# Kernel tuning notes

Measured on AMD Instinct MI355X. Metric: run time of the kernel, lower is better.

Reference implementation:

```python
import jax, jax.numpy as jnp
import numpy as np

B, N, T, D, DG, DS, NC = 16, 64, 256, 64, 64, 9, 2

def _pe(times, d, max_len):
    # PositionalEncodingTF: timescales = max_len ** linspace(0,1,d//2)
    ts = jnp.asarray(max_len ** np.linspace(0.0, 1.0, d // 2), jnp.float32)
    st = times[..., None] / ts
    return jnp.concatenate([jnp.sin(st), jnp.cos(st)], -1)

def _ln(h, g, b):
    m = h.mean(-1, keepdims=True)
    v = ((h - m) ** 2).mean(-1, keepdims=True)
    return (h - m) * jax.lax.rsqrt(v + 1e-5) * g + b

def setup_inputs():
    key = jax.random.key(0)
    ks = jax.random.split(key, 40)
    s = 0.02
    value = jax.random.normal(ks[0], (B, T, N))
    obs = (jax.random.uniform(ks[1], (B, T, N)) < 0.5).astype(jnp.float32)
    times = jnp.sort(jax.random.uniform(ks[2], (B, T)) * T, axis=1)
    F = D + 2 * DG  # per-node GRU input feature size [x_t, h, time_enc]
    return dict(
        x=jnp.concatenate([value, obs, times[..., None]], -1),
        nufft=jax.random.normal(ks[3], (B, 2, T, N)),
        delta_t=jax.random.uniform(ks[4], (B, T)) * 0.1,
        static=jax.random.normal(ks[5], (B, DS)),
        lengths=jax.random.randint(ks[6], (B,), 1, T + 1),
        proj_w=jax.random.normal(ks[7], (2, D)) * s, proj_b=jnp.zeros(D),
        Wqkv=jax.random.normal(ks[8], (D, 3 * D)) * s, bqkv=jnp.zeros(3 * D),
        Wo=jax.random.normal(ks[9], (D, D)) * s, bo=jnp.zeros(D),
        ln1_g=jnp.ones(D), ln1_b=jnp.zeros(D),
        W1=jax.random.normal(ks[10], (D, D)) * s, b1=jnp.zeros(D),
        W2=jax.random.normal(ks[11], (D, D)) * s, b2=jnp.zeros(D),
        ln2_g=jnp.ones(D), ln2_b=jnp.zeros(D),
        WQ_f=jax.random.normal(ks[12], (T, T)) * 0.05,
        WK_f=jax.random.normal(ks[13], (T, T)) * 0.05,
        Wz=jax.random.normal(ks[14], (2 * F, DG)) * s, bz=jnp.zeros(DG),
        Wr=jax.random.normal(ks[15], (2 * F, DG)) * s, br=jnp.zeros(DG),
        Wc=jax.random.normal(ks[16], (2 * F, DG)) * s, bc=jnp.zeros(DG),
        Wfin=jax.random.normal(ks[17], (DG,)) * s, bfin=jnp.zeros(()),
        We=jax.random.normal(ks[18], (DS, N)) * s, be=jnp.zeros(N),
        Wc1=jax.random.normal(ks[19], (2 * N, 200)) * s, bc1=jnp.zeros(200),
        Wc2=jax.random.normal(ks[20], (200, NC)) * s, bc2=jnp.zeros(NC),
    )

def _forward(x, nufft, delta_t, static, lengths, proj_w, proj_b, Wqkv, bqkv, Wo, bo,
             ln1_g, ln1_b, W1, b1, W2, b2, ln2_g, ln2_b, WQ_f, WK_f,
             Wz, bz, Wr, br, Wc, bc, Wfin, bfin, We, be, Wc1, bc1, Wc2, bc2):
    lengths = jnp.maximum(lengths, 1)
    value = x[:, :, :N].transpose(0, 2, 1)          # (B,N,T)
    obs = x[:, :, N:2 * N].transpose(0, 2, 1)       # (B,N,T) observation mask
    times = x[:, :, -1]                              # (B,T)
    # Conv2d(2->D, 1x1) input projection == per-element linear over [value, mask]
    feat = jnp.stack([value, obs], -1) @ proj_w + proj_b   # (B,N,T,D)
    pe1 = _pe(times, D, T)                           # (B,T,D)
    tin = feat + pe1[:, None]                        # (B,N,T,D)
    # single-head transformer encoder layer (post-norm, relu FFN, eval: no dropout)
    qkv = tin @ Wqkv + bqkv
    q, k, v = jnp.split(qkv, 3, -1)
    scores = jnp.einsum('bnqd,bnkd->bnqk', q, k) / jnp.sqrt(jnp.float32(D))
    kpad = jnp.arange(T)[None, :] >= lengths[:, None]      # (B,T) key padding
    scores = jnp.where(kpad[:, None, None, :], -1e9, scores)
    attn = jax.nn.softmax(scores, -1)
    ao = jnp.einsum('bnqk,bnkd->bnqd', attn, v) @ Wo + bo
    h1 = _ln(tin + ao, ln1_g, ln1_b)
    ff = jax.nn.relu(h1 @ W1 + b1) @ W2 + b2
    tout = _ln(h1 + ff, ln2_g, ln2_b)
    m = obs[..., None]
    x_tat = m * tin + (1.0 - m) * tout               # masked blend (B,N,T,D)
    # Variable_Attention_layer on nufft channel 1: relu-score softmax attention
    xf = nufft[:, 1].transpose(0, 2, 1)              # (B,N,T)
    S = jax.nn.relu(jnp.einsum('bnt,bmt->bnm', xf @ WQ_f, xf @ WK_f)) / jnp.sqrt(jnp.float32(T))
    A = jax.nn.softmax(S, -1).mean(0)                # (N,N)
    A = 0.5 * (A + A.T)
    sm = jax.nn.softmax(A, -1)
    A = 0.5 * (sm + sm.T)
    pe2 = _pe(times, DG, T)                          # (B,T,DG)
    # graph-conv GRU over time (CGRNN) with delta_t decay + length masking
    def stepf(h, inputs):
        xt, tet, dtt, t = inputs                     # (B,N,D),(B,DG),(B,),()
        h = h * jnp.exp(-jax.nn.relu(dtt))[:, None, None]
        te = jnp.broadcast_to(tet[:, None, :], (h.shape[0], N, DG))
        inp = jnp.concatenate([xt, h, te], -1)
        gin = jnp.concatenate([inp, jnp.einsum('nm,bmf->bnf', A, inp)], -1)
        z = jax.nn.sigmoid(gin @ Wz + bz)
        r = jax.nn.sigmoid(gin @ Wr + br)
        inc = jnp.concatenate([xt, r * h, te], -1)
        cin = jnp.concatenate([inc, jnp.einsum('nm,bmf->bnf', A, inc)], -1)
        c = jnp.tanh(cin @ Wc + bc)
        hn = z * h + (1.0 - z) * c
        h = jnp.where((t < lengths)[:, None, None], hn, h)
        return h, None
    h0 = jnp.zeros((x.shape[0], N, DG), x.dtype)
    xs = (x_tat.transpose(2, 0, 1, 3), pe2.transpose(1, 0, 2), delta_t.T, jnp.arange(T))
    hT, _ = jax.lax.scan(stepf, h0, xs)
    out = hT @ Wfin + bfin                           # final 1x1 conv -> (B,N)
    emb = static @ We + be                           # (B,N)
    hcl = jax.nn.relu(jnp.concatenate([out, emb], -1) @ Wc1 + bc1)
    return hcl @ Wc2 + bc2                           # (B,NC)

def reference(x, nufft, delta_t, static, lengths, proj_w, proj_b, Wqkv, bqkv, Wo, bo,
              ln1_g, ln1_b, W1, b1, W2, b2, ln2_g, ln2_b, WQ_f, WK_f,
              Wz, bz, Wr, br, Wc, bc, Wfin, bfin, We, be, Wc1, bc1, Wc2, bc2):
    return _forward(x, nufft, delta_t, static, lengths, proj_w, proj_b, Wqkv, bqkv, Wo, bo,
                    ln1_g, ln1_b, W1, b1, W2, b2, ln2_g, ln2_b, WQ_f, WK_f,
                    Wz, bz, Wr, br, Wc, bc, Wfin, bfin, We, be, Wc1, bc1, Wc2, bc2)
```

## Files before the change

### kernel.cpp

```cpp
#include <hip/hip_runtime.h>
#include <hip/hip_bf16.h>
#include <cmath>

#define DEV __device__ __forceinline__

typedef short s16x8 __attribute__((ext_vector_type(8)));
typedef short s16x4 __attribute__((ext_vector_type(4)));
typedef float f32x4 __attribute__((ext_vector_type(4)));

DEV unsigned short f2bu(float x){
  __hip_bfloat16 h = __float2bfloat16(x);
  return *reinterpret_cast<unsigned short*>(&h);
}
DEV float bs2f(unsigned short v){ return __uint_as_float(((unsigned)v)<<16); }
DEV float bs2f(short v){ return bs2f((unsigned short)v); }

DEV int swzo(int row, int col){
  return (row*128 + ((col*2) ^ ((row&7)<<4))) >> 1;
}
DEV s16x8 ldfrag(const short* tile, int t16, int lane, int kk){
  int row = t16 + (lane & 15);
  int c0  = (kk<<5) + ((lane>>4)<<3);
  int off = (row*128 + ((c0<<1) ^ ((row&7)<<4))) >> 1;
  return *(const s16x8*)(tile + off);
}
DEV int swzv(int d, int t){
  return (d*512 + ((t*2) ^ ((d&7)<<4))) >> 1;
}

__global__ void k0_prep(const float* __restrict__ Wqkv, const float* __restrict__ Wo,
                        const float* __restrict__ W1, const float* __restrict__ W2,
                        const float* __restrict__ Wz, const float* __restrict__ Wr,
                        const float* __restrict__ Wc,
                        short* __restrict__ Wqkv_t, short* __restrict__ Wo_t,
                        short* __restrict__ W1_t, short* __restrict__ W2_t,
                        short* __restrict__ Wg_t)
{
  int t = blockIdx.x*256 + threadIdx.x;
  if (t < 12288){ int nn=t>>6, k=t&63; Wqkv_t[t]=(short)f2bu(Wqkv[k*192+nn]); }
  else if (t < 16384){ int e=t-12288; int nn=e>>6,k=e&63; Wo_t[e]=(short)f2bu(Wo[k*64+nn]); }
  else if (t < 20480){ int e=t-16384; int nn=e>>6,k=e&63; W1_t[e]=(short)f2bu(W1[k*64+nn]); }
  else if (t < 24576){ int e=t-20480; int nn=e>>6,k=e&63; W2_t[e]=(short)f2bu(W2[k*64+nn]); }
  else if (t < 49152){
    int e=t-24576;
    int g=e>>13, rem=e&8191, s=rem>>12, rem2=rem&4095, c=rem2>>6, k=rem2&63;
    const float* Wg = (g==0)?Wz:((g==1)?Wr:Wc);
    Wg_t[e] = (short)f2bu(Wg[((s?192:0)+k)*64 + c]);
  }
}

__global__ void k1_pe_u(const float* __restrict__ x, const float* __restrict__ delta_t,
                        const float* __restrict__ Wz, const float* __restrict__ bz,
                        const float* __restrict__ Wr, const float* __restrict__ br,
                        const float* __restrict__ Wc, const float* __restrict__ bc,
                        float* __restrict__ pe, float* __restrict__ U, float* __restrict__ decay)
{
  const int bt = blockIdx.x;
  const int d  = threadIdx.x;
  __shared__ float pes[64];
  float tmv = x[(size_t)bt*129 + 128];
  int j = d & 31;
  float ts = exp2f((float)j * (8.0f/31.0f));
  float st = tmv / ts;
  float v = (d < 32) ? sinf(st) : cosf(st);
  pes[d] = v;
  pe[(size_t)bt*64 + d] = v;
  __syncthreads();
  float a0=bz[d], a1=0.f, a2=br[d], a3=0.f, a4=bc[d], a5=0.f;
  for (int k=0;k<64;k++){
    float p = pes[k];
    a0 = fmaf(p, Wz[(128+k)*64+d], a0);
    a1 = fmaf(p, Wz[(320+k)*64+d], a1);
    a2 = fmaf(p, Wr[(128+k)*64+d], a2);
    a3 = fmaf(p, Wr[(320+k)*64+d], a3);
    a4 = fmaf(p, Wc[(128+k)*64+d], a4);
    a5 = fmaf(p, Wc[(320+k)*64+d], a5);
  }
  float* u = U + (size_t)bt*384;
  u[d]=a0; u[64+d]=a1; u[128+d]=a2; u[192+d]=a3; u[256+d]=a4; u[320+d]=a5;
  if (d==0) decay[bt] = expf(-fmaxf(delta_t[bt], 0.f));
}

__global__ void k2a_qfkf(const float* __restrict__ nufft, const float* __restrict__ WQf,
                         const float* __restrict__ WKf, float* __restrict__ qf, float* __restrict__ kf)
{
  const int bn = blockIdx.x, b = bn>>6, n = bn&63;
  const int u = threadIdx.x;
  __shared__ float xs[256];
  xs[u] = nufft[ ((((size_t)b*2)+1)*256 + u)*64 + n ];
  __syncthreads();
  float aq=0.f, ak=0.f;
  for (int t=0;t<256;t++){
    float xv = xs[t];
    aq = fmaf(xv, WQf[t*256+u], aq);
    ak = fmaf(xv, WKf[t*256+u], ak);
  }
  qf[(size_t)bn*256+u]=aq;
  kf[(size_t)bn*256+u]=ak;
}

__launch_bounds__(256, 1)
__global__ void k2b_soft(const float* __restrict__ qf, const float* __restrict__ kf,
                         float* __restrict__ soft)
{
  const int b = blockIdx.x, tid = threadIdx.x;
  __shared__ float qs[64*257];
  __shared__ float ksh[64*257];
  __shared__ float Ss[64*65];
  const float* qb = qf + ((size_t)b<<14);
  const float* kb = kf + ((size_t)b<<14);
  for (int e=tid; e<16384; e+=256){
    int r=e>>8, c=e&255;
    qs[r*257+c]=qb[e];
    ksh[r*257+c]=kb[e];
  }
  __syncthreads();
  const int n = tid>>2, m0 = (tid&3)<<4;
  float acc[16];
  #pragma unroll
  for (int i=0;i<16;i++) acc[i]=0.f;
  for (int t=0;t<256;t++){
    float qv = qs[n*257+t];
    #pragma unroll
    for (int i=0;i<16;i++) acc[i] = fmaf(qv, ksh[(m0+i)*257+t], acc[i]);
  }
  #pragma unroll
  for (int i=0;i<16;i++) Ss[n*65+m0+i] = fmaxf(acc[i],0.f)*(1.f/16.f);
  __syncthreads();
  if (tid < 64){
    float mx=-1e30f;
    for (int m=0;m<64;m++) mx=fmaxf(mx, Ss[tid*65+m]);
    float s=0.f;
    for (int m=0;m<64;m++) s += expf(Ss[tid*65+m]-mx);
    float inv=1.f/s;
    for (int m=0;m<64;m++) soft[((size_t)b<<12)+(tid<<6)+m] = expf(Ss[tid*65+m]-mx)*inv;
  }
}

__global__ void k2c_A(const float* __restrict__ soft, short* __restrict__ Abf,
                      float* __restrict__ rs_out)
{
  const int tid = threadIdx.x;
  __shared__ float A0[64*65];
  __shared__ float A1[64*65];
  for (int e=tid; e<4096; e+=256){
    int nn=e>>6, mm=e&63;
    float s=0.f;
    #pragma unroll
    for (int b=0;b<16;b++) s += soft[((size_t)b<<12)+e];
    A0[nn*65+mm] = s*(1.f/16.f);
  }
  __syncthreads();
  for (int e=tid; e<4096; e+=256){
    int nn=e>>6, mm=e&63;
    A1[nn*65+mm] = 0.5f*(A0[nn*65+mm]+A0[mm*65+nn]);
  }
  __syncthreads();
  if (tid < 64){
    float mx=-1e30f;
    for (int m=0;m<64;m++) mx=fmaxf(mx, A1[tid*65+m]);
    float s=0.f;
    for (int m=0;m<64;m++) s += expf(A1[tid*65+m]-mx);
    float inv=1.f/s;
    for (int m=0;m<64;m++) A0[tid*65+m] = expf(A1[tid*65+m]-mx)*inv;
  }
  __syncthreads();
  for (int e=tid; e<4096; e+=256){
    int nn=e>>6, mm=e&63;
    float a = 0.5f*(A0[nn*65+mm]+A0[mm*65+nn]);
    A1[nn*65+mm] = a;
    Abf[e] = (short)f2bu(a);
  }
  __syncthreads();
  if (tid < 64){
    float s=0.f;
    for (int m=0;m<64;m++) s += A1[tid*65+m];
    rs_out[tid]=s;
  }
}

__launch_bounds__(512, 1)
__global__ void k3_former(const float* __restrict__ x, const float* __restrict__ pe_g,
    const float* __restrict__ proj_w, const float* __restrict__ proj_b,
    const short* __restrict__ Wqkv_t, const float* __restrict__ bqkv,
    const short* __restrict__ Wo_t, const float* __restrict__ bo,
    const float* __restrict__ ln1g, const float* __restrict__ ln1b,
    const short* __restrict__ W1_t, const float* __restrict__ b1,
    const short* __restrict__ W2_t, const float* __restrict__ b2,
    const float* __restrict__ ln2g, const float* __restrict__ ln2b,
    const int* __restrict__ lengths, unsigned short* __restrict__ xtat)
{
  const int bn = blockIdx.x, b = bn>>6, n = bn&63;
  const int tid = threadIdx.x, w = tid>>6, lane = tid&63;
  const int l15 = lane&15, lhi = lane>>4;
  __shared__ short tp_s[16384];
  __shared__ short q_s[16384];
  __shared__ short k_s[16384];
  __shared__ short v_t[16384];
  __shared__ float valr[256], obsr[256];

// ... 125 lines not shown
      v += __shfl_xor(v,1); v += __shfl_xor(v,2); v += __shfl_xor(v,4); v += __shfl_xor(v,8);
      inv[j][i]=1.f/v;
    }

  #pragma unroll
  for (int j=0;j<2;j++){
    const int rt=w+(j<<3);
    if (rt < LT){
      const int rb=(rt<<4)+(lhi<<2);
      #pragma unroll
      for (int dt=0;dt<4;dt++)
        #pragma unroll
        for (int i=0;i<4;i++)
          q_s[swzo(rb+i,(dt<<4)+l15)] = (short)f2bu(Oac[j][dt][i]*inv[j][i]);
    }
  }
  __syncthreads();

  f32x4 h1[2][4];
  #pragma unroll
  for (int j=0;j<2;j++){
    const int rt=w+(j<<3);
    if (rt < LT){
      s16x8 a0=ldfrag(q_s, rt<<4, lane, 0);
      s16x8 a1=ldfrag(q_s, rt<<4, lane, 1);
      const int rb=(rt<<4)+(lhi<<2);
      #pragma unroll
      for (int dt=0;dt<4;dt++){
        const int col=(dt<<4)+l15;
        const short* wb = Wo_t + (col<<6) + (lhi<<3);
        s16x8 b0=*(const s16x8*)wb, b1v=*(const s16x8*)(wb+32);
        float bias=bo[col];
        f32x4 acc={bias,bias,bias,bias};
        acc=__builtin_amdgcn_mfma_f32_16x16x32_bf16(a0,b0,acc,0,0,0);
        acc=__builtin_amdgcn_mfma_f32_16x16x32_bf16(a1,b1v,acc,0,0,0);
        #pragma unroll
        for(int i=0;i<4;i++){
          const int row=rb+i;
          acc[i]+= fmaf(valr[row],proj_w[col], fmaf(obsr[row],proj_w[64+col], proj_b[col]))
                 + pe_g[(((size_t)b<<8)+row)*64+col];
        }
        h1[j][dt]=acc;
      }
      f32x4 mu, rsq;
      #pragma unroll
      for(int i=0;i<4;i++){
        float sv = h1[j][0][i]+h1[j][1][i]+h1[j][2][i]+h1[j][3][i];
        sv += __shfl_xor(sv,1); sv+=__shfl_xor(sv,2); sv+=__shfl_xor(sv,4); sv+=__shfl_xor(sv,8);
        mu[i]=sv*(1.f/64.f);
      }
      #pragma unroll
      for(int i=0;i<4;i++){
        float sv=0.f;
        #pragma unroll
        for(int dt=0;dt<4;dt++){ float c=h1[j][dt][i]-mu[i]; sv=fmaf(c,c,sv); }
        sv += __shfl_xor(sv,1); sv+=__shfl_xor(sv,2); sv+=__shfl_xor(sv,4); sv+=__shfl_xor(sv,8);
        rsq[i]=1.f/sqrtf(sv*(1.f/64.f)+1e-5f);
      }
      #pragma unroll
      for(int dt=0;dt<4;dt++){
        const int col=(dt<<4)+l15;
        float g=ln1g[col], bb=ln1b[col];
        #pragma unroll
        for(int i=0;i<4;i++){
          float hv=(h1[j][dt][i]-mu[i])*rsq[i]*g+bb;
          h1[j][dt][i]=hv;
          k_s[swzo(rb+i,col)] = (short)f2bu(hv);
        }
      }
    }
  }
  __syncthreads();

  #pragma unroll
  for (int j=0;j<2;j++){
    const int rt=w+(j<<3);
    if (rt < LT){
      s16x8 a0=ldfrag(k_s, rt<<4, lane, 0);
      s16x8 a1=ldfrag(k_s, rt<<4, lane, 1);
      const int rb=(rt<<4)+(lhi<<2);
      #pragma unroll
      for (int dt=0;dt<4;dt++){
        const int col=(dt<<4)+l15;
        const short* wb = W1_t + (col<<6)+(lhi<<3);
        s16x8 b0=*(const s16x8*)wb, b1v=*(const s16x8*)(wb+32);
        float bias=b1[col];
        f32x4 acc={bias,bias,bias,bias};
        acc=__builtin_amdgcn_mfma_f32_16x16x32_bf16(a0,b0,acc,0,0,0);
        acc=__builtin_amdgcn_mfma_f32_16x16x32_bf16(a1,b1v,acc,0,0,0);
        #pragma unroll
        for(int i=0;i<4;i++) tp_s[swzo(rb+i,col)]=(short)f2bu(fmaxf(acc[i],0.f));
      }
    }
  }
  __syncthreads();

  #pragma unroll
  for (int j=0;j<2;j++){
    const int rt=w+(j<<3);
    if (rt < LT){
      s16x8 a0=ldfrag(tp_s, rt<<4, lane, 0);
      s16x8 a1=ldfrag(tp_s, rt<<4, lane, 1);
      const int rb=(rt<<4)+(lhi<<2);
      f32x4 to[4];
      #pragma unroll
      for (int dt=0;dt<4;dt++){
        const int col=(dt<<4)+l15;
        const short* wb = W2_t + (col<<6)+(lhi<<3);
        s16x8 b0=*(const s16x8*)wb, b1v=*(const s16x8*)(wb+32);
        float bias=b2[col];
        f32x4 acc={bias,bias,bias,bias};
        acc=__builtin_amdgcn_mfma_f32_16x16x32_bf16(a0,b0,acc,0,0,0);
        acc=__builtin_amdgcn_mfma_f32_16x16x32_bf16(a1,b1v,acc,0,0,0);
        acc += h1[j][dt];
        to[dt]=acc;
      }
      f32x4 mu, rsq;
      #pragma unroll
      for(int i=0;i<4;i++){
        float sv = to[0][i]+to[1][i]+to[2][i]+to[3][i];
        sv += __shfl_xor(sv,1); sv+=__shfl_xor(sv,2); sv+=__shfl_xor(sv,4); sv+=__shfl_xor(sv,8);
        mu[i]=sv*(1.f/64.f);
      }
      #pragma unroll
      for(int i=0;i<4;i++){
        float sv=0.f;
        #pragma unroll
        for(int dt=0;dt<4;dt++){ float c=to[dt][i]-mu[i]; sv=fmaf(c,c,sv); }
        sv += __shfl_xor(sv,1); sv+=__shfl_xor(sv,2); sv+=__shfl_xor(sv,4); sv+=__shfl_xor(sv,8);
        rsq[i]=1.f/sqrtf(sv*(1.f/64.f)+1e-5f);
      }
      #pragma unroll
      for(int dt=0;dt<4;dt++){
        const int col=(dt<<4)+l15;
        float g=ln2g[col], bb=ln2b[col];
        #pragma unroll
        for(int i=0;i<4;i++){
          const int row=rb+i;
          if (row < len){
            float tv=(to[dt][i]-mu[i])*rsq[i]*g+bb;
            float tin = fmaf(valr[row],proj_w[col], fmaf(obsr[row],proj_w[64+col], proj_b[col]))
                      + pe_g[(((size_t)b<<8)+row)*64+col];
            float ob = obsr[row];
            xtat[((size_t)bn<<14)+(row<<6)+col] = f2bu(ob*tin + (1.f-ob)*tv);
          }
        }
      }
    }
  }
}

__global__ void k35_xg(const unsigned short* __restrict__ xtat, const short* __restrict__ Abf,
                       const short* __restrict__ Wg_t, const int* __restrict__ lengths,
                       unsigned short* __restrict__ Xall)
{
  const int bt = blockIdx.x, b = bt>>8, t = bt&255;
  int len = lengths[b]; if (len<1) len=1;
  if (t >= len) return;
  const int tid = threadIdx.x, w = tid>>6, lane = tid&63;
  const int l15 = lane&15, lhi = lane>>4;
  __shared__ short xt_rm[4096], xt_tp[4096], axt_rm[4096];

  #pragma unroll
  for (int q=0;q<2;q++){
    int e = tid + (q<<8);
    int nn = e>>3, c0 = (e&7)<<3;
    s16x8 v = *(const s16x8*)((const short*)xtat + (((size_t)(b*64+nn)*256 + t)<<6) + c0);
    *(s16x8*)(xt_rm + swzo(nn,c0)) = v;
    #pragma unroll
    for (int jj=0;jj<8;jj++) xt_tp[swzo(c0+jj, nn)] = v[jj];
  }
  __syncthreads();

  {
    s16x8 bx[2];
    #pragma unroll
    for (int kk=0;kk<2;kk++) bx[kk]=ldfrag(xt_tp, w<<4, lane, kk);
    #pragma unroll
    for (int rt=0;rt<4;rt++){
      f32x4 acc={0.f,0.f,0.f,0.f};
      #pragma unroll
      for (int kk=0;kk<2;kk++){
        s16x8 af = *(const s16x8*)(Abf + ((rt<<4)+l15)*64 + (kk<<5) + (lhi<<3));
        acc=__builtin_amdgcn_mfma_f32_16x16x32_bf16(af,bx[kk],acc,0,0,0);
      }
      const int rb=(rt<<4)+(lhi<<2);
      #pragma unroll
      for(int i=0;i<4;i++) axt_rm[swzo(rb+i,(w<<4)+l15)] = (short)f2bu(acc[i]);
    }
  }
  __syncthreads();

  s16x8 fx[4][2], fa[4][2];
  #pragma unroll
  for (int rt=0;rt<4;rt++)
    #pragma unroll
    for (int kk=0;kk<2;kk++){
      fx[rt][kk]=ldfrag(xt_rm, rt<<4, lane, kk);
      fa[rt][kk]=ldfrag(axt_rm, rt<<4, lane, kk);
    }
  const int col = (w<<4)+l15;
  #pragma unroll
  for (int g=0; g<3; g++){
    s16x8 wbx[2], wba[2];
    #pragma unroll
    for (int kk=0;kk<2;kk++){
      wbx[kk] = *(const s16x8*)(Wg_t + (((g<<1)  )*64 + col)*64 + (kk<<5)+(lhi<<3));
      wba[kk] = *(const s16x8*)(Wg_t + (((g<<1)+1)*64 + col)*64 + (kk<<5)+(lhi<<3));
    }
    #pragma unroll
    for (int rt=0;rt<4;rt++){
      f32x4 acc={0.f,0.f,0.f,0.f};
      #pragma unroll
      for (int kk=0;kk<2;kk++){
        acc=__builtin_amdgcn_mfma_f32_16x16x32_bf16(fx[rt][kk],wbx[kk],acc,0,0,0);
        acc=__builtin_amdgcn_mfma_f32_16x16x32_bf16(fa[rt][kk],wba[kk],acc,0,0,0);
      }
      s16x4 pk;
      #pragma unroll
      for(int i=0;i<4;i++) pk[i]=(short)f2bu(acc[i]);
      *(s16x4*)((short*)Xall + ((size_t)(bt*3+g)<<12) + (col<<6) + (rt<<4)+(lhi<<2)) = pk;
    }
  }
}

__launch_bounds__(512, 1)
__global__ void k4_scan(const unsigned short* __restrict__ Xall, const float* __restrict__ U,
                        const float* __restrict__ decay, const short* __restrict__ Abf,
                        const float* __restrict__ rs_g,
                        const float* __restrict__ Wz, const float* __restrict__ Wr,
                        const float* __restrict__ Wc,
                        const int* __restrict__ lengths, float* __restrict__ hT)
{
  const int b = blockIdx.x;
  const int tid = threadIdx.x;
  const int w = tid >> 6, lane = tid & 63;
  const int tn = w & 3, tm0 = (w >> 2) << 1;
  const int l15 = lane & 15, lhi = lane >> 4;
  const int colg = (tn<<4) + l15;
  const int rsub = lhi << 2;

  __shared__ short h_rm[4096], h_tp[4096], rh_rm[4096], rh_tp[4096];
  __shared__ short ah_rm[4096], arh_rm[4096];
  __shared__ float dec_s[256];

  int len = lengths[b]; if (len < 1) len = 1;
  for (int e=tid; e<256; e+=512) dec_s[e] = decay[b*256+e];

  int rb0 = (tm0<<4) + rsub, rb1 = ((tm0+1)<<4) + rsub;
  f32x4 rs4[2];
  rs4[0] = *(const f32x4*)(rs_g + rb0);
  rs4[1] = *(const f32x4*)(rs_g + rb1);

  s16x8 aA[2][2];
  #pragma unroll
  for (int ti=0;ti<2;ti++)
    #pragma unroll
    for (int kk=0;kk<2;kk++)
      aA[ti][kk] = *(const s16x8*)(Abf + (((tm0+ti)<<4) + l15)*64 + (kk<<5) + (lhi<<3));

  s16x8 wf[3][2][2];
  {
    const float* Wg[3] = {Wz, Wr, Wc};
    #pragma unroll
    for (int g=0; g<3; g++)
      #pragma unroll
      for (int s=0; s<2; s++)
        #pragma unroll
        for (int kk=0; kk<2; kk++){
          s16x8 tf;
          int kb = (kk<<5) + (lhi<<3);
          #pragma unroll
          for (int j=0;j<8;j++)
            tf[j] = (short)f2bu(Wg[g][((s?256:64)+kb+j)*64 + colg]);
          wf[g][s][kk] = tf;
        }
  }

  f32x4 hreg[2] = {{0.f,0.f,0.f,0.f},{0.f,0.f,0.f,0.f}};

  const short* Xb = (const short*)Xall + ((size_t)(b*256)*3<<12);
  s16x4 xc[6]; float uc[6];
  {
    const short* xp = Xb;
    #pragma unroll
    for (int g=0;g<3;g++){
      xc[g*2+0] = *(const s16x4*)(xp + ((size_t)g<<12) + (colg<<6) + rb0);
      xc[g*2+1] = *(const s16x4*)(xp + ((size_t)g<<12) + (colg<<6) + rb1);
    }
    const float* ub = U + (size_t)(b*256)*384;
    #pragma unroll
    for (int q=0;q<6;q++) uc[q] = ub[q*64 + colg];
  }
  __syncthreads();

  for (int t=0; t<len; t++){
    float dc = dec_s[t];
    #pragma unroll
    for (int ti=0;ti<2;ti++)
      #pragma unroll
      for (int i=0;i<4;i++) hreg[ti][i] *= dc;

    #pragma unroll
    for (int ti=0;ti<2;ti++){
      int rb = ti ? rb1 : rb0;
      s16x4 hp;
      #pragma unroll
      for (int i=0;i<4;i++){
        short hv = (short)f2bu(hreg[ti][i]);
        h_rm[swzo(rb+i, colg)] = hv;
        hp[i] = hv;
      }
      *(s16x4*)(h_tp + swzo(colg, rb)) = hp;
    }

    s16x4 xn[6]; float un[6];
    #pragma unroll
    for (int q=0;q<6;q++){ xn[q]=(s16x4){0,0,0,0}; un[q]=0.f; }
    if (t+1 < len){
      const short* xp = Xb + ((size_t)(t+1)*3<<12);
      #pragma unroll
      for (int g=0;g<3;g++){
        xn[g*2+0] = *(const s16x4*)(xp + ((size_t)g<<12) + (colg<<6) + rb0);
        xn[g*2+1] = *(const s16x4*)(xp + ((size_t)g<<12) + (colg<<6) + rb1);
      }
      const float* ub = U + (size_t)(b*256+t+1)*384;
      #pragma unroll
      for (int q=0;q<6;q++) un[q] = ub[q*64 + colg];
    }
    __syncthreads();

    {
      f32x4 ah[2] = {{0,0,0,0},{0,0,0,0}};
      #pragma unroll
      for (int kk=0;kk<2;kk++){
        s16x8 bh = ldfrag(h_tp, tn<<4, lane, kk);
        #pragma unroll
        for (int ti=0;ti<2;ti++)
          ah[ti] = __builtin_amdgcn_mfma_f32_16x16x32_bf16(aA[ti][kk], bh, ah[ti], 0,0,0);
      }
      #pragma unroll
      for (int ti=0;ti<2;ti++){
        int rb = ti ? rb1 : rb0;
        #pragma unroll
        for (int i=0;i<4;i++) ah_rm[swzo(rb+i, colg)] = (short)f2bu(ah[ti][i]);
      }
    }
    __syncthreads();

    f32x4 zz[2];
    #pragma unroll
    for (int ti=0;ti<2;ti++){
      int rt = (tm0+ti)<<4;
      int rb = ti ? rb1 : rb0;
      f32x4 gz, gr;
      #pragma unroll
      for (int i=0;i<4;i++){
        gz[i] = bs2f(xc[ti][i])   + uc[0] + rs4[ti][i]*uc[1];
        gr[i] = bs2f(xc[2+ti][i]) + uc[2] + rs4[ti][i]*uc[3];
      }
      #pragma unroll
      for (int kk=0;kk<2;kk++){
        s16x8 fh = ldfrag(h_rm,  rt, lane, kk);
        s16x8 fa = ldfrag(ah_rm, rt, lane, kk);
        gz = __builtin_amdgcn_mfma_f32_16x16x32_bf16(fh, wf[0][0][kk], gz, 0,0,0);
        gz = __builtin_amdgcn_mfma_f32_16x16x32_bf16(fa, wf[0][1][kk], gz, 0,0,0);
        gr = __builtin_amdgcn_mfma_f32_16x16x32_bf16(fh, wf[1][0][kk], gr, 0,0,0);
        gr = __builtin_amdgcn_mfma_f32_16x16x32_bf16(fa, wf[1][1][kk], gr, 0,0,0);
      }
      s16x4 rhp;
      #pragma unroll
      for (int i=0;i<4;i++){
        float zv = 1.f/(1.f+__expf(-gz[i]));
        float rv = 1.f/(1.f+__expf(-gr[i]));
        zz[ti][i] = zv;
        short rhv = (short)f2bu(rv * hreg[ti][i]);
        rh_rm[swzo(rb+i, colg)] = rhv;
        rhp[i] = rhv;
      }
      *(s16x4*)(rh_tp + swzo(colg, rb)) = rhp;
    }
    __syncthreads();

    {
      f32x4 ar[2] = {{0,0,0,0},{0,0,0,0}};
      #pragma unroll
      for (int kk=0;kk<2;kk++){
        s16x8 brh = ldfrag(rh_tp, tn<<4, lane, kk);
        #pragma unroll
        for (int ti=0;ti<2;ti++)
          ar[ti] = __builtin_amdgcn_mfma_f32_16x16x32_bf16(aA[ti][kk], brh, ar[ti], 0,0,0);
      }
      #pragma unroll
      for (int ti=0;ti<2;ti++){
        int rb = ti ? rb1 : rb0;
        #pragma unroll
        for (int i=0;i<4;i++) arh_rm[swzo(rb+i, colg)] = (short)f2bu(ar[ti][i]);
      }
    }
    __syncthreads();

    #pragma unroll
    for (int ti=0;ti<2;ti++){
      int rt = (tm0+ti)<<4;
      f32x4 gc;
      #pragma unroll
      for (int i=0;i<4;i++)
        gc[i] = bs2f(xc[4+ti][i]) + uc[4] + rs4[ti][i]*uc[5];
      #pragma unroll
      for (int kk=0;kk<2;kk++){
        s16x8 frh = ldfrag(rh_rm,  rt, lane, kk);
        s16x8 far = ldfrag(arh_rm, rt, lane, kk);
        gc = __builtin_amdgcn_mfma_f32_16x16x32_bf16(frh, wf[2][0][kk], gc, 0,0,0);
        gc = __builtin_amdgcn_mfma_f32_16x16x32_bf16(far, wf[2][1][kk], gc, 0,0,0);
      }
      #pragma unroll
      for (int i=0;i<4;i++){
        float cv = 1.f - 2.f/(__expf(2.f*gc[i])+1.f);
        float zv = zz[ti][i];
        hreg[ti][i] = zv*hreg[ti][i] + (1.f-zv)*cv;
      }
    }

    #pragma unroll
    for (int q=0;q<6;q++){ xc[q]=xn[q]; uc[q]=un[q]; }
  }

  float sp = 1.f;
  for (int t=len; t<256; t++) sp *= dec_s[t];
  #pragma unroll
  for (int ti=0;ti<2;ti++)
    #pragma unroll
    for (int i=0;i<4;i++) hreg[ti][i] *= sp;

  #pragma unroll
  for (int ti=0;ti<2;ti++){
    int rb = ti ? rb1 : rb0;
    #pragma unroll
    for (int i=0;i<4;i++)
      hT[(((size_t)b<<6) + rb + i)*64 + colg] = hreg[ti][i];
  }
}

__global__ void k5_head(const float* __restrict__ hT, const float* __restrict__ Wfin,
                        const float* __restrict__ bfin,
                        const float* __restrict__ stat, const float* __restrict__ We,
                        const float* __restrict__ be,
                        const float* __restrict__ Wc1, const float* __restrict__ bc1,
                        const float* __restrict__ Wc2, const float* __restrict__ bc2,
                        float* __restrict__ out)
{
  const int b = blockIdx.x, tid = threadIdx.x;
  __shared__ float cat[128];
  __shared__ float hcl[200];
  if (tid < 64){
    const float* hr = hT + (((size_t)b<<6)+tid)*64;
    float a = bfin[0];
    #pragma unroll
    for (int d=0;d<64;d++) a = fmaf(hr[d], Wfin[d], a);
    cat[tid]=a;
  } else if (tid < 128){
    int nn = tid-64;
    float a = be[nn];
    #pragma unroll
    for (int k=0;k<9;k++) a = fmaf(stat[b*9+k], We[k*64+nn], a);
    cat[tid]=a;
  }
  __syncthreads();
  if (tid < 200){
    float a = bc1[tid];
    for (int k=0;k<128;k++) a = fmaf(cat[k], Wc1[k*200+tid], a);
    hcl[tid] = fmaxf(a, 0.f);
  }
  __syncthreads();
  if (tid < 2){
    float a = bc2[tid];
    for (int k=0;k<200;k++) a = fmaf(hcl[k], Wc2[k*2+tid], a);
    out[b*2+tid] = a;
  }
}

extern "C" void kernel_launch(void* const* d_in, const int* in_sizes, int n_in,
                              void* d_out, int out_size, void* d_ws, size_t ws_size,
                              hipStream_t stream)
{
  const float* x       = (const float*)d_in[0];
  const float* nufft   = (const float*)d_in[1];
  const float* delta_t = (const float*)d_in[2];
  const float* stat    = (const float*)d_in[3];
  const int*   lengths = (const int*)  d_in[4];
  const float* proj_w  = (const float*)d_in[5];
  const float* proj_b  = (const float*)d_in[6];
  const float* Wqkv    = (const float*)d_in[7];
  const float* bqkv    = (const float*)d_in[8];
  const float* Wo      = (const float*)d_in[9];
  const float* bo      = (const float*)d_in[10];
  const float* ln1g    = (const float*)d_in[11];
  const float* ln1b    = (const float*)d_in[12];
  const float* W1      = (const float*)d_in[13];
  const float* b1      = (const float*)d_in[14];
  const float* W2      = (const float*)d_in[15];
  const float* b2      = (const float*)d_in[16];
  const float* ln2g    = (const float*)d_in[17];
  const float* ln2b    = (const float*)d_in[18];
  const float* WQf     = (const float*)d_in[19];
  const float* WKf     = (const float*)d_in[20];
  const float* Wz      = (const float*)d_in[21];
  const float* bz      = (const float*)d_in[22];
  const float* Wr      = (const float*)d_in[23];
  const float* br      = (const float*)d_in[24];
  const float* Wc      = (const float*)d_in[25];
  const float* bc      = (const float*)d_in[26];
  const float* Wfin    = (const float*)d_in[27];
  const float* bfin    = (const float*)d_in[28];
  const float* We      = (const float*)d_in[29];
  const float* be      = (const float*)d_in[30];
  const float* Wc1     = (const float*)d_in[31];
  const float* bc1     = (const float*)d_in[32];
  const float* Wc2     = (const float*)d_in[33];
  const float* bc2     = (const float*)d_in[34];
  float* out = (float*)d_out;

  char* ws = (char*)d_ws;
  size_t o = 0;
  float* pe    = (float*)(ws+o); o += (size_t)4096*64*4;
  float* U     = (float*)(ws+o); o += (size_t)4096*384*4;
  float* decay = (float*)(ws+o); o += (size_t)4096*4;
  unsigned short* xtat = (unsigned short*)(ws+o); o += (size_t)1024*256*64*2;
  float* qf    = (float*)(ws+o); o += (size_t)1024*256*4;
  float* kf    = (float*)(ws+o); o += (size_t)1024*256*4;
  float* soft  = (float*)(ws+o); o += (size_t)16*4096*4;
  short* Abf   = (short*)(ws+o); o += (size_t)4096*2;
  float* rs    = (float*)(ws+o); o += (size_t)64*4;
  float* hT    = (float*)(ws+o); o += (size_t)16*64*64*4;
  short* Wqkv_t= (short*)(ws+o); o += (size_t)12288*2;
  short* Wo_t  = (short*)(ws+o); o += (size_t)4096*2;
  short* W1_t  = (short*)(ws+o); o += (size_t)4096*2;
  short* W2_t  = (short*)(ws+o); o += (size_t)4096*2;
  short* Wg_t  = (short*)(ws+o); o += (size_t)24576*2;
  unsigned short* Xall = (unsigned short*)(ws+o); o += (size_t)4096*3*4096*2;
  (void)ws_size; (void)in_sizes; (void)n_in; (void)out_size;

  hipLaunchKernelGGL(k0_prep,   dim3(192),  dim3(256), 0, stream,
                     Wqkv, Wo, W1, W2, Wz, Wr, Wc, Wqkv_t, Wo_t, W1_t, W2_t, Wg_t);
  hipLaunchKernelGGL(k1_pe_u,   dim3(4096), dim3(64),  0, stream,
                     x, delta_t, Wz, bz, Wr, br, Wc, bc, pe, U, decay);
  hipLaunchKernelGGL(k2a_qfkf,  dim3(1024), dim3(256), 0, stream,
                     nufft, WQf, WKf, qf, kf);
  hipLaunchKernelGGL(k2b_soft,  dim3(16),   dim3(256), 0, stream, qf, kf, soft);
  hipLaunchKernelGGL(k2c_A,     dim3(1),    dim3(256), 0, stream, soft, Abf, rs);
  hipLaunchKernelGGL(k3_former, dim3(1024), dim3(512), 0, stream,
                     x, pe, proj_w, proj_b, Wqkv_t, bqkv, Wo_t, bo, ln1g, ln1b,
                     W1_t, b1, W2_t, b2, ln2g, ln2b, lengths, xtat);
  hipLaunchKernelGGL(k35_xg,    dim3(4096), dim3(256), 0, stream,
                     xtat, Abf, Wg_t, lengths, Xall);
  hipLaunchKernelGGL(k4_scan,   dim3(16),   dim3(512), 0, stream,
                     Xall, U, decay, Abf, rs, Wz, Wr, Wc, lengths, hT);
  hipLaunchKernelGGL(k5_head,   dim3(16),   dim3(256), 0, stream,
                     hT, Wfin, bfin, stat, We, be, Wc1, bc1, Wc2, bc2, out);
}
```

Before: 1.072 ms.

## Restructure GRU scan work split, fold U bias into Xall, prebuild bf16 h-weights

The sequential scan kernel gets a new wave-to-tile mapping: each wave owns one 16-row node tile and two 16-column feature tiles, with precomputed swizzled LDS offsets, DPP lane swaps plus packed bf16 conversion for stores, and lighter barriers that only wait on LDS. The per-step U and row-sum bias terms move into the parallel k35_xg kernel, which removes per-step U loads from the serial loop. Hidden-state weights are converted to bf16 once in k0_prep instead of being gathered and converted per block. The aim is a shorter serial critical path per timestep. In exchange there is more inline asm and DPP lane-swap logic, and folding the bias into Xall before bf16 rounding changes precision slightly.

```diff
diff --git a/kernel.cpp b/kernel.cpp
--- a/kernel.cpp
+++ b/kernel.cpp
@@ -7,6 +7,7 @@
 typedef short s16x8 __attribute__((ext_vector_type(8)));
 typedef short s16x4 __attribute__((ext_vector_type(4)));
 typedef float f32x4 __attribute__((ext_vector_type(4)));
+typedef int   i32x2 __attribute__((ext_vector_type(2)));
 
 DEV unsigned short f2bu(float x){
   __hip_bfloat16 h = __float2bfloat16(x);
@@ -14,6 +15,20 @@
 }
 DEV float bs2f(unsigned short v){ return __uint_as_float(((unsigned)v)<<16); }
 DEV float bs2f(short v){ return bs2f((unsigned short)v); }
+
+DEV unsigned cvtpk(float lo, float hi){
+  unsigned r;
+  asm("v_cvt_pk_bf16_f32 %0, %1, %2" : "=v"(r) : "v"(lo), "v"(hi));
+  return r;
+}
+DEV float dppx1(float v){
+  int r = __builtin_amdgcn_mov_dpp(__float_as_int(v), 0xB1, 0xF, 0xF, true);
+  return __int_as_float(r);
+}
+
+#define BAR() do { asm volatile("s_waitcnt lgkmcnt(0)" ::: "memory"); \
+                   __builtin_amdgcn_s_barrier(); \
+                   __builtin_amdgcn_sched_barrier(0); } while(0)
 
 DEV int swzo(int row, int col){
   return (row*128 + ((col*2) ^ ((row&7)<<4))) >> 1;
@@ -34,7 +49,7 @@
                         const float* __restrict__ Wc,
                         short* __restrict__ Wqkv_t, short* __restrict__ Wo_t,
                         short* __restrict__ W1_t, short* __restrict__ W2_t,
-                        short* __restrict__ Wg_t)
+                        short* __restrict__ Wg_t, short* __restrict__ Wg_h)
 {
   int t = blockIdx.x*256 + threadIdx.x;
   if (t < 12288){ int nn=t>>6, k=t&63; Wqkv_t[t]=(short)f2bu(Wqkv[k*192+nn]); }
@@ -46,6 +61,12 @@
     int g=e>>13, rem=e&8191, s=rem>>12, rem2=rem&4095, c=rem2>>6, k=rem2&63;
     const float* Wg = (g==0)?Wz:((g==1)?Wr:Wc);
     Wg_t[e] = (short)f2bu(Wg[((s?192:0)+k)*64 + c]);
+  }
+  else if (t < 73728){
+    int e=t-49152;
+    int g=e>>13, rem=e&8191, s=rem>>12, rem2=rem&4095, c=rem2>>6, k=rem2&63;
+    const float* Wg = (g==0)?Wz:((g==1)?Wr:Wc);
+    Wg_h[e] = (short)f2bu(Wg[((s?256:64)+k)*64 + c]);
   }
 }
 
@@ -477,6 +498,7 @@
 
 __global__ void k35_xg(const unsigned short* __restrict__ xtat, const short* __restrict__ Abf,
                        const short* __restrict__ Wg_t, const int* __restrict__ lengths,
+                       const float* __restrict__ U, const float* __restrict__ rs_g,
                        unsigned short* __restrict__ Xall)
 {
   const int bt = blockIdx.x, b = bt>>8, t = bt&255;
@@ -524,18 +546,24 @@
       fx[rt][kk]=ldfrag(xt_rm, rt<<4, lane, kk);
       fa[rt][kk]=ldfrag(axt_rm, rt<<4, lane, kk);
     }
-  const int col = (w<<4)+l15;
+  const int dcol = (w<<4)+l15;
+  f32x4 rsv[4];
+  #pragma unroll
+  for (int rt=0;rt<4;rt++) rsv[rt] = *(const f32x4*)(rs_g + (rt<<4) + (lhi<<2));
+  const float* Ub = U + (size_t)bt*384;
   #pragma unroll
   for (int g=0; g<3; g++){
     s16x8 wbx[2], wba[2];
     #pragma unroll
     for (int kk=0;kk<2;kk++){
-      wbx[kk] = *(const s16x8*)(Wg_t + (((g<<1)  )*64 + col)*64 + (kk<<5)+(lhi<<3));
-      wba[kk] = *(const s16x8*)(Wg_t + (((g<<1)+1)*64 + col)*64 + (kk<<5)+(lhi<<3));
-    }
+      wbx[kk] = *(const s16x8*)(Wg_t + (((g<<1)  )*64 + dcol)*64 + (kk<<5)+(lhi<<3));
+      wba[kk] = *(const s16x8*)(Wg_t + (((g<<1)+1)*64 + dcol)*64 + (kk<<5)+(lhi<<3));
+    }
+    float u1 = Ub[(g<<7) + dcol];
+    float u2 = Ub[(g<<7) + 64 + dcol];
     #pragma unroll
     for (int rt=0;rt<4;rt++){
-      f32x4 acc={0.f,0.f,0.f,0.f};
+      f32x4 acc={u1,u1,u1,u1};
       #pragma unroll
       for (int kk=0;kk<2;kk++){
         acc=__builtin_amdgcn_mfma_f32_16x16x32_bf16(fx[rt][kk],wbx[kk],acc,0,0,0);
@@ -543,228 +571,248 @@
       }
       s16x4 pk;
       #pragma unroll
-      for(int i=0;i<4;i++) pk[i]=(short)f2bu(acc[i]);
-      *(s16x4*)((short*)Xall + ((size_t)(bt*3+g)<<12) + (col<<6) + (rt<<4)+(lhi<<2)) = pk;
+      for(int i=0;i<4;i++) pk[i]=(short)f2bu(acc[i] + rsv[rt][i]*u2);
+      *(s16x4*)((short*)Xall + (((size_t)bt*3 + g)*64 + dcol)*64 + (rt<<4)+(lhi<<2)) = pk;
     }
   }
 }
 
 __launch_bounds__(512, 1)
-__global__ void k4_scan(const unsigned short* __restrict__ Xall, const float* __restrict__ U,
+__global__ void k4_scan(const unsigned short* __restrict__ Xall,
                         const float* __restrict__ decay, const short* __restrict__ Abf,
-                        const float* __restrict__ rs_g,
-                        const float* __restrict__ Wz, const float* __restrict__ Wr,
-                        const float* __restrict__ Wc,
+                        const short* __restrict__ Wg_h,
                         const int* __restrict__ lengths, float* __restrict__ hT)
 {
-  const int b = blockIdx.x;
-  const int tid = threadIdx.x;
-  const int w = tid >> 6, lane = tid & 63;
-  const int tn = w & 3, tm0 = (w >> 2) << 1;
-  const int l15 = lane & 15, lhi = lane >> 4;
-  const int colg = (tn<<4) + l15;
-  const int rsub = lhi << 2;
-
-  __shared__ short h_rm[4096], h_tp[4096], rh_rm[4096], rh_tp[4096];
-  __shared__ short ah_rm[4096], arh_rm[4096];
+  const int b = blockIdx.x, tid = threadIdx.x;
+  const int w = tid>>6, lane = tid&63;
+  const int l15 = lane&15, lhi = lane>>4;
+  const int pe_ = l15&1;
+  const int rnt = w>>1, dp = w&1;
+  const int nb_ = (rnt<<4) + (lhi<<2);
+  const int d0 = (dp<<5) + l15, d1 = (dp<<5) + 16 + l15;
+  const int tmA0 = (w&1)<<1, tmA1 = tmA0+1;
+  const int dnA = w>>1;
+
+  __shared__ short h_rm[4096], h_tp[4096], ah_rm[4096];
+  __shared__ short rh_rm[4096], rh_tp[4096], arh_rm[4096];
   __shared__ float dec_s[256];
 
-  int len = lengths[b]; if (len < 1) len = 1;
+  int len = lengths[b]; if (len<1) len=1;
   for (int e=tid; e<256; e+=512) dec_s[e] = decay[b*256+e];
 
-  int rb0 = (tm0<<4) + rsub, rb1 = ((tm0+1)<<4) + rsub;
-  f32x4 rs4[2];
-  rs4[0] = *(const f32x4*)(rs_g + rb0);
-  rs4[1] = *(const f32x4*)(rs_g + rb1);
-
   s16x8 aA[2][2];
   #pragma unroll
-  for (int ti=0;ti<2;ti++)
+  for (int t2=0;t2<2;t2++)
     #pragma unroll
     for (int kk=0;kk<2;kk++)
-      aA[ti][kk] = *(const s16x8*)(Abf + (((tm0+ti)<<4) + l15)*64 + (kk<<5) + (lhi<<3));
-
-  s16x8 wf[3][2][2];
+      aA[t2][kk] = *(const s16x8*)(Abf + (((t2?tmA1:tmA0)<<4) + l15)*64 + (kk<<5) + (lhi<<3));
+
+  s16x8 wf[3][2][2][2];
+  #pragma unroll
+  for (int g=0;g<3;g++)
+    #pragma unroll
+    for (int s=0;s<2;s++)
+      #pragma unroll
+      for (int kk=0;kk<2;kk++)
+        #pragma unroll
+        for (int e=0;e<2;e++)
+          wf[g][s][kk][e] = *(const s16x8*)(Wg_h + (((g*2+s)*64 + (e?d1:d0))<<6) + (kk<<5) + (lhi<<3));
+
+  int tpo[2];
+  #pragma unroll
+  for (int e=0;e<2;e++){ int r = e?d1:d0; tpo[e] = r*128 + (((nb_)*2) ^ ((r&7)<<4)); }
+  int rmo[4];
+  { int dPr = ((dp<<1) + pe_)*16 + (l15 & ~1);
+    #pragma unroll
+    for (int i=0;i<4;i++){ int n = nb_+i; rmo[i] = n*128 + ((dPr*2) ^ ((n&7)<<4)); } }
+  int amo[4];
+  { int dAr = (dnA<<4) + (l15 & ~1);
+    int tb = (pe_? tmA1 : tmA0)<<4;
+    #pragma unroll
+    for (int i=0;i<4;i++){ int n = tb + (lhi<<2) + i; amo[i] = n*128 + ((dAr*2) ^ ((n&7)<<4)); } }
+  int rdT[2], rdR[2];
+  { int r = (dnA<<4)+l15;
+    #pragma unroll
+    for (int kk=0;kk<2;kk++) rdT[kk] = r*128 + (((kk<<6) + (lhi<<4)) ^ ((r&7)<<4)); }
+  { int r = (rnt<<4)+l15;
+    #pragma unroll
+    for (int kk=0;kk<2;kk++) rdR[kk] = r*128 + (((kk<<6) + (lhi<<4)) ^ ((r&7)<<4)); }
+
+  f32x4 hreg[2] = {{0.f,0.f,0.f,0.f},{0.f,0.f,0.f,0.f}};
+  f32x4 zz[2];
+
+  const short* Xb = (const short*)Xall;
+  s16x4 xzc[2], xrc[2], xcc[2], xzn[2], xrn[2], xcn[2];
+  #pragma unroll
+  for (int e=0;e<2;e++){ xzc[e]=(s16x4){0,0,0,0}; xrc[e]=xzc[e]; xcc[e]=xzc[e]; }
   {
-    const float* Wg[3] = {Wz, Wr, Wc};
-    #pragma unroll
-    for (int g=0; g<3; g++)
-      #pragma unroll
-      for (int s=0; s<2; s++)
-        #pragma unroll
-        for (int kk=0; kk<2; kk++){
-          s16x8 tf;
-          int kb = (kk<<5) + (lhi<<3);
-          #pragma unroll
-          for (int j=0;j<8;j++)
-            tf[j] = (short)f2bu(Wg[g][((s?256:64)+kb+j)*64 + colg]);
-          wf[g][s][kk] = tf;
-        }
-  }
-
-  f32x4 hreg[2] = {{0.f,0.f,0.f,0.f},{0.f,0.f,0.f,0.f}};
-
-  const short* Xb = (const short*)Xall + ((size_t)(b*256)*3<<12);
-  s16x4 xc[6]; float uc[6];
-  {
-    const short* xp = Xb;
-    #pragma unroll
-    for (int g=0;g<3;g++){
-      xc[g*2+0] = *(const s16x4*)(xp + ((size_t)g<<12) + (colg<<6) + rb0);
-      xc[g*2+1] = *(const s16x4*)(xp + ((size_t)g<<12) + (colg<<6) + rb1);
-    }
-    const float* ub = U + (size_t)(b*256)*384;
-    #pragma unroll
-    for (int q=0;q<6;q++) uc[q] = ub[q*64 + colg];
+    const short* base = Xb + ((size_t)(b*256))*12288;
+    #pragma unroll
+    for (int e=0;e<2;e++){
+      int de = e?d1:d0;
+      xzc[e] = *(const s16x4*)(base + (0*64 + de)*64 + nb_);
+      xrc[e] = *(const s16x4*)(base + (1*64 + de)*64 + nb_);
+      xcc[e] = *(const s16x4*)(base + (2*64 + de)*64 + nb_);
+    }
   }
   __syncthreads();
 
   for (int t=0; t<len; t++){
     float dc = dec_s[t];
     #pragma unroll
-    for (int ti=0;ti<2;ti++)
-      #pragma unroll
-      for (int i=0;i<4;i++) hreg[ti][i] *= dc;
-
-    #pragma unroll
-    for (int ti=0;ti<2;ti++){
-      int rb = ti ? rb1 : rb0;
-      s16x4 hp;
+    for (int e=0;e<2;e++)
+      #pragma unroll
+      for (int i=0;i<4;i++) hreg[e][i] *= dc;
+
+    #pragma unroll
+    for (int e=0;e<2;e++){ xzn[e]=(s16x4){0,0,0,0}; xrn[e]=xzn[e]; xcn[e]=xzn[e]; }
+    if (t+1 < len){
+      const short* base = Xb + ((size_t)(b*256 + t+1))*12288;
+      #pragma unroll
+      for (int e=0;e<2;e++){
+        int de = e?d1:d0;
+        xzn[e] = *(const s16x4*)(base + (0*64 + de)*64 + nb_);
+        xrn[e] = *(const s16x4*)(base + (1*64 + de)*64 + nb_);
+        xcn[e] = *(const s16x4*)(base + (2*64 + de)*64 + nb_);
+      }
+    }
+
+    #pragma unroll
+    for (int e=0;e<2;e++){
+      i32x2 v; v[0] = (int)cvtpk(hreg[e][0], hreg[e][1]);
+               v[1] = (int)cvtpk(hreg[e][2], hreg[e][3]);
+      *(i32x2*)((char*)h_tp + tpo[e]) = v;
+    }
+    #pragma unroll
+    for (int i=0;i<4;i++){
+      float v0 = hreg[0][i], v1 = hreg[1][i];
+      float n0 = dppx1(v0), n1 = dppx1(v1);
+      float lo = pe_ ? n1 : v0;
+      float hi = pe_ ? v1 : n0;
+      *(unsigned*)((char*)h_rm + rmo[i]) = cvtpk(lo, hi);
+    }
+    BAR();
+
+    {
+      s16x8 bh0 = *(const s16x8*)((const char*)h_tp + rdT[0]);
+      s16x8 bh1 = *(const s16x8*)((const char*)h_tp + rdT[1]);
+      f32x4 a0v={0.f,0.f,0.f,0.f}, a1v={0.f,0.f,0.f,0.f};
+      a0v = __builtin_amdgcn_mfma_f32_16x16x32_bf16(aA[0][0], bh0, a0v, 0,0,0);
+      a0v = __builtin_amdgcn_mfma_f32_16x16x32_bf16(aA[0][1], bh1, a0v, 0,0,0);
+      a1v = __builtin_amdgcn_mfma_f32_16x16x32_bf16(aA[1][0], bh0, a1v, 0,0,0);
+      a1v = __builtin_amdgcn_mfma_f32_16x16x32_bf16(aA[1][1], bh1, a1v, 0,0,0);
       #pragma unroll
       for (int i=0;i<4;i++){
-        short hv = (short)f2bu(hreg[ti][i]);
-        h_rm[swzo(rb+i, colg)] = hv;
-        hp[i] = hv;
-      }
-      *(s16x4*)(h_tp + swzo(colg, rb)) = hp;
-    }
-
-    s16x4 xn[6]; float un[6];
-    #pragma unroll
-    for (int q=0;q<6;q++){ xn[q]=(s16x4){0,0,0,0}; un[q]=0.f; }
-    if (t+1 < len){
-      const short* xp = Xb + ((size_t)(t+1)*3<<12);
-      #pragma unroll
-      for (int g=0;g<3;g++){
-        xn[g*2+0] = *(const s16x4*)(xp + ((size_t)g<<12) + (colg<<6) + rb0);
-        xn[g*2+1] = *(const s16x4*)(xp + ((size_t)g<<12) + (colg<<6) + rb1);
-      }
-      const float* ub = U + (size_t)(b*256+t+1)*384;
-      #pragma unroll
-      for (int q=0;q<6;q++) un[q] = ub[q*64 + colg];
-    }
-    __syncthreads();
+        float n0 = dppx1(a0v[i]), n1 = dppx1(a1v[i]);
+        float lo = pe_ ? n1 : a0v[i];
+        float hi = pe_ ? a1v[i] : n0;
+        *(unsigned*)((char*)ah_rm + amo[i]) = cvtpk(lo, hi);
+      }
+    }
+    BAR();
 
     {
-      f32x4 ah[2] = {{0,0,0,0},{0,0,0,0}};
-      #pragma unroll
-      for (int kk=0;kk<2;kk++){
-        s16x8 bh = ldfrag(h_tp, tn<<4, lane, kk);
-        #pragma unroll
-        for (int ti=0;ti<2;ti++)
-          ah[ti] = __builtin_amdgcn_mfma_f32_16x16x32_bf16(aA[ti][kk], bh, ah[ti], 0,0,0);
-      }
-      #pragma unroll
-      for (int ti=0;ti<2;ti++){
-        int rb = ti ? rb1 : rb0;
-        #pragma unroll
-        for (int i=0;i<4;i++) ah_rm[swzo(rb+i, colg)] = (short)f2bu(ah[ti][i]);
-      }
-    }
-    __syncthreads();
-
-    f32x4 zz[2];
-    #pragma unroll
-    for (int ti=0;ti<2;ti++){
-      int rt = (tm0+ti)<<4;
-      int rb = ti ? rb1 : rb0;
-      f32x4 gz, gr;
+      s16x8 fh0 = *(const s16x8*)((const char*)h_rm  + rdR[0]);
+      s16x8 fh1 = *(const s16x8*)((const char*)h_rm  + rdR[1]);
+      s16x8 fa0 = *(const s16x8*)((const char*)ah_rm + rdR[0]);
+      s16x8 fa1 = *(const s16x8*)((const char*)ah_rm + rdR[1]);
+      f32x4 gz[2], gr[2], rh[2];
+      #pragma unroll
+      for (int e=0;e<2;e++)
+        #pragma unroll
+        for (int i=0;i<4;i++){ gz[e][i]=bs2f(xzc[e][i]); gr[e][i]=bs2f(xrc[e][i]); }
+      #pragma unroll
+      for (int e=0;e<2;e++){
+        gz[e] = __builtin_amdgcn_mfma_f32_16x16x32_bf16(fh0, wf[0][0][0][e], gz[e], 0,0,0);
+        gz[e] = __builtin_amdgcn_mfma_f32_16x16x32_bf16(fh1, wf[0][0][1][e], gz[e], 0,0,0);
+        gz[e] = __builtin_amdgcn_mfma_f32_16x16x32_bf16(fa0, wf[0][1][0][e], gz[e], 0,0,0);
+        gz[e] = __builtin_amdgcn_mfma_f32_16x16x32_bf16(fa1, wf[0][1][1][e], gz[e], 0,0,0);
+        gr[e] = __builtin_amdgcn_mfma_f32_16x16x32_bf16(fh0, wf[1][0][0][e], gr[e], 0,0,0);
+        gr[e] = __builtin_amdgcn_mfma_f32_16x16x32_bf16(fh1, wf[1][0][1][e], gr[e], 0,0,0);
+        gr[e] = __builtin_amdgcn_mfma_f32_16x16x32_bf16(fa0, wf[1][1][0][e], gr[e], 0,0,0);
+        gr[e] = __builtin_amdgcn_mfma_f32_16x16x32_bf16(fa1, wf[1][1][1][e], gr[e], 0,0,0);
+      }
+      #pragma unroll
+      for (int e=0;e<2;e++)
+        #pragma unroll
+        for (int i=0;i<4;i++){
+          float zv = 1.f/(1.f+__expf(-gz[e][i]));
+          float rv = 1.f/(1.f+__expf(-gr[e][i]));
+          zz[e][i] = zv;
+          rh[e][i] = rv * hreg[e][i];
+        }
+      #pragma unroll
+      for (int e=0;e<2;e++){
+        i32x2 v; v[0] = (int)cvtpk(rh[e][0], rh[e][1]);
+                 v[1] = (int)cvtpk(rh[e][2], rh[e][3]);
+        *(i32x2*)((char*)rh_tp + tpo[e]) = v;
+      }
       #pragma unroll
       for (int i=0;i<4;i++){
-        gz[i] = bs2f(xc[ti][i])   + uc[0] + rs4[ti][i]*uc[1];
-        gr[i] = bs2f(xc[2+ti][i]) + uc[2] + rs4[ti][i]*uc[3];
-      }
-      #pragma unroll
-      for (int kk=0;kk<2;kk++){
-        s16x8 fh = ldfrag(h_rm,  rt, lane, kk);
-        s16x8 fa = ldfrag(ah_rm, rt, lane, kk);
-        gz = __builtin_amdgcn_mfma_f32_16x16x32_bf16(fh, wf[0][0][kk], gz, 0,0,0);
-        gz = __builtin_amdgcn_mfma_f32_16x16x32_bf16(fa, wf[0][1][kk], gz, 0,0,0);
-        gr = __builtin_amdgcn_mfma_f32_16x16x32_bf16(fh, wf[1][0][kk], gr, 0,0,0);
-        gr = __builtin_amdgcn_mfma_f32_16x16x32_bf16(fa, wf[1][1][kk], gr, 0,0,0);
-      }
-      s16x4 rhp;
+        float v0 = rh[0][i], v1 = rh[1][i];
+        float n0 = dppx1(v0), n1 = dppx1(v1);
+        float lo = pe_ ? n1 : v0;
+        float hi = pe_ ? v1 : n0;
+        *(unsigned*)((char*)rh_rm + rmo[i]) = cvtpk(lo, hi);
+      }
+    }
+    BAR();
+
+    {
+      s16x8 br0 = *(const s16x8*)((const char*)rh_tp + rdT[0]);
+      s16x8 br1 = *(const s16x8*)((const char*)rh_tp + rdT[1]);
+      f32x4 a0v={0.f,0.f,0.f,0.f}, a1v={0.f,0.f,0.f,0.f};
+      a0v = __builtin_amdgcn_mfma_f32_16x16x32_bf16(aA[0][0], br0, a0v, 0,0,0);
+      a0v = __builtin_amdgcn_mfma_f32_16x16x32_bf16(aA[0][1], br1, a0v, 0,0,0);
+      a1v = __builtin_amdgcn_mfma_f32_16x16x32_bf16(aA[1][0], br0, a1v, 0,0,0);
+      a1v = __builtin_amdgcn_mfma_f32_16x16x32_bf16(aA[1][1], br1, a1v, 0,0,0);
       #pragma unroll
       for (int i=0;i<4;i++){
-        float zv = 1.f/(1.f+__expf(-gz[i]));
-        float rv = 1.f/(1.f+__expf(-gr[i]));
-        zz[ti][i] = zv;
-        short rhv = (short)f2bu(rv * hreg[ti][i]);
-        rh_rm[swzo(rb+i, colg)] = rhv;
-        rhp[i] = rhv;
-      }
-      *(s16x4*)(rh_tp + swzo(colg, rb)) = rhp;
-    }
-    __syncthreads();
+        float n0 = dppx1(a0v[i]), n1 = dppx1(a1v[i]);
+        float lo = pe_ ? n1 : a0v[i];
+        float hi = pe_ ? a1v[i] : n0;
+        *(unsigned*)((char*)arh_rm + amo[i]) = cvtpk(lo, hi);
+      }
+    }
+    BAR();
 
     {
-      f32x4 ar[2] = {{0,0,0,0},{0,0,0,0}};
-      #pragma unroll
-      for (int kk=0;kk<2;kk++){
-        s16x8 brh = ldfrag(rh_tp, tn<<4, lane, kk);
-        #pragma unroll
-        for (int ti=0;ti<2;ti++)
-          ar[ti] = __builtin_amdgcn_mfma_f32_16x16x32_bf16(aA[ti][kk], brh, ar[ti], 0,0,0);
-      }
-      #pragma unroll
-      for (int ti=0;ti<2;ti++){
-        int rb = ti ? rb1 : rb0;
-        #pragma unroll
-        for (int i=0;i<4;i++) arh_rm[swzo(rb+i, colg)] = (short)f2bu(ar[ti][i]);
-      }
-    }
-    __syncthreads();
-
-    #pragma unroll
-    for (int ti=0;ti<2;ti++){
-      int rt = (tm0+ti)<<4;
-      f32x4 gc;
-      #pragma unroll
-      for (int i=0;i<4;i++)
-        gc[i] = bs2f(xc[4+ti][i]) + uc[4] + rs4[ti][i]*uc[5];
-      #pragma unroll
-      for (int kk=0;kk<2;kk++){
-        s16x8 frh = ldfrag(rh_rm,  rt, lane, kk);
-        s16x8 far = ldfrag(arh_rm, rt, lane, kk);
-        gc = __builtin_amdgcn_mfma_f32_16x16x32_bf16(frh, wf[2][0][kk], gc, 0,0,0);
-        gc = __builtin_amdgcn_mfma_f32_16x16x32_bf16(far, wf[2][1][kk], gc, 0,0,0);
-      }
-      #pragma unroll
-      for (int i=0;i<4;i++){
-        float cv = 1.f - 2.f/(__expf(2.f*gc[i])+1.f);
-        float zv = zz[ti][i];
-        hreg[ti][i] = zv*hreg[ti][i] + (1.f-zv)*cv;
-      }
-    }
-
-    #pragma unroll
-    for (int q=0;q<6;q++){ xc[q]=xn[q]; uc[q]=un[q]; }
+      s16x8 fr0 = *(const s16x8*)((const char*)rh_rm  + rdR[0]);
+      s16x8 fr1 = *(const s16x8*)((const char*)rh_rm  + rdR[1]);
+      s16x8 fb0 = *(const s16x8*)((const char*)arh_rm + rdR[0]);
+      s16x8 fb1 = *(const s16x8*)((const char*)arh_rm + rdR[1]);
+      f32x4 gc[2];
+      #pragma unroll
+      for (int e=0;e<2;e++)
+        #pragma unroll
+        for (int i=0;i<4;i++) gc[e][i]=bs2f(xcc[e][i]);
+      #pragma unroll
+      for (int e=0;e<2;e++){
+        gc[e] = __builtin_amdgcn_mfma_f32_16x16x32_bf16(fr0, wf[2][0][0][e], gc[e], 0,0,0);
+        gc[e] = __builtin_amdgcn_mfma_f32_16x16x32_bf16(fr1, wf[2][0][1][e], gc[e], 0,0,0);
+        gc[e] = __builtin_amdgcn_mfma_f32_16x16x32_bf16(fb0, wf[2][1][0][e], gc[e], 0,0,0);
+        gc[e] = __builtin_amdgcn_mfma_f32_16x16x32_bf16(fb1, wf[2][1][1][e], gc[e], 0,0,0);
+      }
+      #pragma unroll
+      for (int e=0;e<2;e++)
+        #pragma unroll
+        for (int i=0;i<4;i++){
+          float cv = 1.f - 2.f/(__expf(2.f*gc[e][i])+1.f);
+          hreg[e][i] = fmaf(zz[e][i], hreg[e][i]-cv, cv);
+        }
+    }
+
+    #pragma unroll
+    for (int e=0;e<2;e++){ xzc[e]=xzn[e]; xrc[e]=xrn[e]; xcc[e]=xcn[e]; }
   }
 
   float sp = 1.f;
   for (int t=len; t<256; t++) sp *= dec_s[t];
   #pragma unroll
-  for (int ti=0;ti<2;ti++)
-    #pragma unroll
-    for (int i=0;i<4;i++) hreg[ti][i] *= sp;
-
-  #pragma unroll
-  for (int ti=0;ti<2;ti++){
-    int rb = ti ? rb1 : rb0;
+  for (int e=0;e<2;e++)
     #pragma unroll
     for (int i=0;i<4;i++)
-      hT[(((size_t)b<<6) + rb + i)*64 + colg] = hreg[ti][i];
-  }
+      hT[(((size_t)b<<6) + nb_ + i)*64 + (e?d1:d0)] = hreg[e][i]*sp;
 }
 
 __global__ void k5_head(const float* __restrict__ hT, const float* __restrict__ Wfin,
@@ -863,11 +911,12 @@
   short* W1_t  = (short*)(ws+o); o += (size_t)4096*2;
   short* W2_t  = (short*)(ws+o); o += (size_t)4096*2;
   short* Wg_t  = (short*)(ws+o); o += (size_t)24576*2;
+  short* Wg_h  = (short*)(ws+o); o += (size_t)24576*2;
   unsigned short* Xall = (unsigned short*)(ws+o); o += (size_t)4096*3*4096*2;
   (void)ws_size; (void)in_sizes; (void)n_in; (void)out_size;
 
-  hipLaunchKernelGGL(k0_prep,   dim3(192),  dim3(256), 0, stream,
-                     Wqkv, Wo, W1, W2, Wz, Wr, Wc, Wqkv_t, Wo_t, W1_t, W2_t, Wg_t);
+  hipLaunchKernelGGL(k0_prep,   dim3(288),  dim3(256), 0, stream,
+                     Wqkv, Wo, W1, W2, Wz, Wr, Wc, Wqkv_t, Wo_t, W1_t, W2_t, Wg_t, Wg_h);
   hipLaunchKernelGGL(k1_pe_u,   dim3(4096), dim3(64),  0, stream,
                      x, delta_t, Wz, bz, Wr, br, Wc, bc, pe, U, decay);
   hipLaunchKernelGGL(k2a_qfkf,  dim3(1024), dim3(256), 0, stream,
@@ -878,9 +927,9 @@
                      x, pe, proj_w, proj_b, Wqkv_t, bqkv, Wo_t, bo, ln1g, ln1b,
                      W1_t, b1, W2_t, b2, ln2g, ln2b, lengths, xtat);
   hipLaunchKernelGGL(k35_xg,    dim3(4096), dim3(256), 0, stream,
-                     xtat, Abf, Wg_t, lengths, Xall);
+                     xtat, Abf, Wg_t, lengths, U, rs, Xall);
   hipLaunchKernelGGL(k4_scan,   dim3(16),   dim3(512), 0, stream,
-                     Xall, U, decay, Abf, rs, Wz, Wr, Wc, lengths, hT);
+                     Xall, decay, Abf, Wg_h, lengths, hT);
   hipLaunchKernelGGL(k5_head,   dim3(16),   dim3(256), 0, stream,
                      hT, Wfin, bfin, stat, We, be, Wc1, bc1, Wc2, bc2, out);
 }
```

Result: faster. 864.9 us (-19.3%).
